# Kernel tuning notes

Hardware: AMD Instinct MI355X
Metric: run time of the kernel (lower is better)

Reference implementation:

```python
import jax, jax.numpy as jnp
import numpy as np

D = 2          # matrix dimension
N = 5_000_000  # chain length (and divisor in I + A_i/n)


def setup_inputs() -> dict:
    key = jax.random.key(0)
    A = jax.random.normal(key, (N, D, D), dtype=jnp.float32)
    return {"A": A}


def reference(A):
    # X = prod_{i=0}^{n-1} (I + A_i / n), left-to-right, exactly as the torch loop.
    n = A.shape[0]
    d = A.shape[1]
    I = jnp.eye(d, dtype=A.dtype)

    def step(X, A_i):
        return X @ (I + A_i / n), None

    X, _ = jax.lax.scan(step, I, A)
    return X
```

## Files before the change

kernel.cpp:

```cpp
#include <hip/hip_runtime.h>


struct M2 { double a, b, c, d; };

__device__ __forceinline__ M2 m2mul(const M2& X, const M2& Y) {
    M2 r;
    r.a = fma(X.a, Y.a, X.b * Y.c);
    r.b = fma(X.a, Y.b, X.b * Y.d);
    r.c = fma(X.c, Y.a, X.d * Y.c);
    r.d = fma(X.c, Y.b, X.d * Y.d);
    return r;
}

__device__ __forceinline__ M2 from_f4(float4 v, double inv_n) {
    M2 M;
    M.a = fma((double)v.x, inv_n, 1.0);
    M.b = (double)v.y * inv_n;
    M.c = (double)v.z * inv_n;
    M.d = fma((double)v.w, inv_n, 1.0);
    return M;
}

__device__ __forceinline__ M2 wave_combine(M2 P) {
    #pragma unroll
    for (int off = 1; off < 64; off <<= 1) {
        M2 Q;
        Q.a = __shfl_down(P.a, off);
        Q.b = __shfl_down(P.b, off);
        Q.c = __shfl_down(P.c, off);
        Q.d = __shfl_down(P.d, off);
        P = m2mul(P, Q);
    }
    return P;
}

__device__ __forceinline__ M2 load_m2(const double* p) {
    double2 lo = *reinterpret_cast<const double2*>(p);
    double2 hi = *reinterpret_cast<const double2*>(p + 2);
    M2 Q = { lo.x, lo.y, hi.x, hi.y };
    return Q;
}

__device__ __forceinline__ void store_m2(double* p, const M2& P) {
    *reinterpret_cast<double2*>(p)     = double2{ P.a, P.b };
    *reinterpret_cast<double2*>(p + 2) = double2{ P.c, P.d };
}

#define CHUNK 5
#define P1_TPB 256
#define WTILE (64 * CHUNK)
#define TILE (P1_TPB * CHUNK)

__global__ void __launch_bounds__(P1_TPB) prodchain_phase1(
    const float4* __restrict__ A, int n, double* __restrict__ part)
{
    __shared__ float4 tile[TILE];
    __shared__ double bl[4 * 4];
    const int tid = threadIdx.x;
    const int w = tid >> 6;
    const int l = tid & 63;
    const int blockStart = blockIdx.x * TILE;
    const int waveStart = blockStart + w * WTILE;
    const double inv_n = 1.0 / (double)n;

    float4* lbase = &tile[w * WTILE];

    if (blockStart + TILE <= n) {
        const float4* gbase = A + waveStart;
        #pragma unroll
        for (int k = 0; k < CHUNK; ++k) {
            __builtin_amdgcn_global_load_lds(
                (const __attribute__((address_space(1))) void*)(gbase + k * 64 + l),
                (__attribute__((address_space(3))) void*)(lbase + k * 64),
                16, 0, 0);
        }
        asm volatile("s_waitcnt vmcnt(0)" ::: "memory");
    } else {
        #pragma unroll
        for (int k = 0; k < CHUNK; ++k) {
            int g = waveStart + k * 64 + l;
            float4 v = (g < n) ? A[g] : make_float4(0.f, 0.f, 0.f, 0.f);
            lbase[k * 64 + l] = v;
        }
    }

    M2 P = {1.0, 0.0, 0.0, 1.0};
    const float4* my = &lbase[l * CHUNK];
    #pragma unroll
    for (int j = 0; j < CHUNK; ++j)
        P = m2mul(P, from_f4(my[j], inv_n));

    P = wave_combine(P);

    if (l == 0) {
        bl[4 * w + 0] = P.a;
        bl[4 * w + 1] = P.b;
        bl[4 * w + 2] = P.c;
        bl[4 * w + 3] = P.d;
    }
    __syncthreads();

    if (tid == 0) {
        M2 R = { bl[0], bl[1], bl[2], bl[3] };
        #pragma unroll
        for (int w2 = 1; w2 < 4; ++w2) {
            M2 Q = { bl[4 * w2 + 0], bl[4 * w2 + 1],
                     bl[4 * w2 + 2], bl[4 * w2 + 3] };
            R = m2mul(R, Q);
        }
        store_m2(&part[4 * blockIdx.x], R);
    }
}

__global__ void __launch_bounds__(64) prodchain_reduce(
    const double* __restrict__ in_part, int np, double* __restrict__ out_part)
{
    const int l = threadIdx.x;
    const int idx = blockIdx.x * 64 + l;
    M2 P = {1.0, 0.0, 0.0, 1.0};
    if (idx < np) P = load_m2(&in_part[4 * idx]);

    P = wave_combine(P);

    if (l == 0) store_m2(&out_part[4 * blockIdx.x], P);
}

__global__ void __launch_bounds__(64) prodchain_final(
    const double* __restrict__ in_part, int np, float* __restrict__ out)
{
    const int l = threadIdx.x;
    M2 P = {1.0, 0.0, 0.0, 1.0};
    if (l < np) P = load_m2(&in_part[4 * l]);

    P = wave_combine(P);

    if (l == 0) {
        out[0] = (float)P.a;
        out[1] = (float)P.b;
        out[2] = (float)P.c;
        out[3] = (float)P.d;
    }
}

extern "C" void kernel_launch(void* const* d_in, const int* in_sizes, int n_in,
                              void* d_out, int out_size, void* d_ws, size_t ws_size,
                              hipStream_t stream) {
    const float4* A = (const float4*)d_in[0];
    const int n = in_sizes[0] / 4;
    const int nb1 = (n + TILE - 1) / TILE;
    const int nb2 = (nb1 + 63) / 64;

    double* part1 = (double*)d_ws;
    double* part2 = part1 + 4 * 4096;

    prodchain_phase1<<<nb1, P1_TPB, 0, stream>>>(A, n, part1);
    prodchain_reduce<<<nb2, 64, 0, stream>>>(part1, nb1, part2);
    prodchain_final<<<1, 64, 0, stream>>>(part2, nb2, (float*)d_out);
}
```

Before: 23.18 us.

## Process two segments per wave, overlapping second load with first compute

Each wave now loads two consecutive 320-element segments into LDS. It waits only for the first batch (vmcnt(5)) before computing that segment's product, so the second batch's load overlaps that arithmetic. The block tile doubles, which halves the number of phase-1 blocks and partials. The small block-reduction scratch is aliased onto the tile buffer behind an extra barrier. The trade-off is fewer blocks in flight for hiding memory latency, plus a second wave-level combine per wave.

```diff
diff --git a/kernel.cpp b/kernel.cpp
--- a/kernel.cpp
+++ b/kernel.cpp
@@ -48,55 +48,85 @@
 
 #define CHUNK 5
 #define P1_TPB 256
-#define WTILE (64 * CHUNK)
-#define TILE (P1_TPB * CHUNK)
+#define SEG (64 * CHUNK)
+#define TILE (SEG * 8)
 
 __global__ void __launch_bounds__(P1_TPB) prodchain_phase1(
     const float4* __restrict__ A, int n, double* __restrict__ part)
 {
     __shared__ float4 tile[TILE];
-    __shared__ double bl[4 * 4];
+    double* bl = (double*)tile;
+
     const int tid = threadIdx.x;
     const int w = tid >> 6;
     const int l = tid & 63;
     const int blockStart = blockIdx.x * TILE;
-    const int waveStart = blockStart + w * WTILE;
+    const int segA = blockStart + (2 * w) * SEG;
+    const int segB = segA + SEG;
     const double inv_n = 1.0 / (double)n;
 
-    float4* lbase = &tile[w * WTILE];
+    float4* la = &tile[(2 * w) * SEG];
+    float4* lb = la + SEG;
 
-    if (blockStart + TILE <= n) {
-        const float4* gbase = A + waveStart;
+    const bool full = (blockStart + TILE <= n);
+    if (full) {
+        const float4* ga = A + segA;
+        const float4* gb = A + segB;
         #pragma unroll
-        for (int k = 0; k < CHUNK; ++k) {
+        for (int k = 0; k < CHUNK; ++k)
             __builtin_amdgcn_global_load_lds(
-                (const __attribute__((address_space(1))) void*)(gbase + k * 64 + l),
-                (__attribute__((address_space(3))) void*)(lbase + k * 64),
+                (const __attribute__((address_space(1))) void*)(ga + k * 64 + l),
+                (__attribute__((address_space(3))) void*)(la + k * 64),
                 16, 0, 0);
-        }
-        asm volatile("s_waitcnt vmcnt(0)" ::: "memory");
+        #pragma unroll
+        for (int k = 0; k < CHUNK; ++k)
+            __builtin_amdgcn_global_load_lds(
+                (const __attribute__((address_space(1))) void*)(gb + k * 64 + l),
+                (__attribute__((address_space(3))) void*)(lb + k * 64),
+                16, 0, 0);
+        asm volatile("s_waitcnt vmcnt(5)" ::: "memory");
     } else {
         #pragma unroll
         for (int k = 0; k < CHUNK; ++k) {
-            int g = waveStart + k * 64 + l;
-            float4 v = (g < n) ? A[g] : make_float4(0.f, 0.f, 0.f, 0.f);
-            lbase[k * 64 + l] = v;
+            int g = segA + k * 64 + l;
+            la[k * 64 + l] = (g < n) ? A[g] : make_float4(0.f, 0.f, 0.f, 0.f);
         }
+        #pragma unroll
+        for (int k = 0; k < CHUNK; ++k) {
+            int g = segB + k * 64 + l;
+            lb[k * 64 + l] = (g < n) ? A[g] : make_float4(0.f, 0.f, 0.f, 0.f);
+        }
+        asm volatile("s_waitcnt lgkmcnt(0)" ::: "memory");
     }
 
     M2 P = {1.0, 0.0, 0.0, 1.0};
-    const float4* my = &lbase[l * CHUNK];
-    #pragma unroll
-    for (int j = 0; j < CHUNK; ++j)
-        P = m2mul(P, from_f4(my[j], inv_n));
+    {
+        const float4* my = &la[l * CHUNK];
+        #pragma unroll
+        for (int j = 0; j < CHUNK; ++j)
+            P = m2mul(P, from_f4(my[j], inv_n));
+    }
+
+    if (full) asm volatile("s_waitcnt vmcnt(0)" ::: "memory");
+
+    M2 Q = {1.0, 0.0, 0.0, 1.0};
+    {
+        const float4* my = &lb[l * CHUNK];
+        #pragma unroll
+        for (int j = 0; j < CHUNK; ++j)
+            Q = m2mul(Q, from_f4(my[j], inv_n));
+    }
 
     P = wave_combine(P);
+    Q = wave_combine(Q);
 
+    __syncthreads();
     if (l == 0) {
-        bl[4 * w + 0] = P.a;
-        bl[4 * w + 1] = P.b;
-        bl[4 * w + 2] = P.c;
-        bl[4 * w + 3] = P.d;
+        M2 R = m2mul(P, Q);
+        bl[4 * w + 0] = R.a;
+        bl[4 * w + 1] = R.b;
+        bl[4 * w + 2] = R.c;
+        bl[4 * w + 3] = R.d;
     }
     __syncthreads();
 
@@ -104,9 +134,9 @@
         M2 R = { bl[0], bl[1], bl[2], bl[3] };
         #pragma unroll
         for (int w2 = 1; w2 < 4; ++w2) {
-            M2 Q = { bl[4 * w2 + 0], bl[4 * w2 + 1],
+            M2 T = { bl[4 * w2 + 0], bl[4 * w2 + 1],
                      bl[4 * w2 + 2], bl[4 * w2 + 3] };
-            R = m2mul(R, Q);
+            R = m2mul(R, T);
         }
         store_m2(&part[4 * blockIdx.x], R);
     }
@@ -151,7 +181,7 @@
     const int nb2 = (nb1 + 63) / 64;
 
     double* part1 = (double*)d_ws;
-    double* part2 = part1 + 4 * 4096;
+    double* part2 = part1 + 4 * 2048;
 
     prodchain_phase1<<<nb1, P1_TPB, 0, stream>>>(A, n, part1);
     prodchain_reduce<<<nb2, 64, 0, stream>>>(part1, nb1, part2);
```

Result: slower. 23.71 us (+2.3%).

## Fuse three-stage product reduction into one kernel with last-block atomic counters

Applied to the files above, without the earlier changes.

Merges the phase1, reduce and final kernels into a single kernel. Each group's last-arriving block, found via an atomic counter, reduces that group's partials, and the last group finisher computes the final product. This removes two kernel launches and their inter-kernel gaps but adds a memset of the counters and relies on relaxed atomics with waitcnt for cross-block visibility, which risks memory-ordering issues.

```diff
diff --git a/kernel.cpp b/kernel.cpp
--- a/kernel.cpp
+++ b/kernel.cpp
@@ -34,16 +34,20 @@
     return P;
 }
 
-__device__ __forceinline__ M2 load_m2(const double* p) {
-    double2 lo = *reinterpret_cast<const double2*>(p);
-    double2 hi = *reinterpret_cast<const double2*>(p + 2);
-    M2 Q = { lo.x, lo.y, hi.x, hi.y };
+__device__ __forceinline__ M2 load_m2_sc1(const double* p) {
+    M2 Q;
+    Q.a = __hip_atomic_load(p + 0, __ATOMIC_RELAXED, __HIP_MEMORY_SCOPE_AGENT);
+    Q.b = __hip_atomic_load(p + 1, __ATOMIC_RELAXED, __HIP_MEMORY_SCOPE_AGENT);
+    Q.c = __hip_atomic_load(p + 2, __ATOMIC_RELAXED, __HIP_MEMORY_SCOPE_AGENT);
+    Q.d = __hip_atomic_load(p + 3, __ATOMIC_RELAXED, __HIP_MEMORY_SCOPE_AGENT);
     return Q;
 }
 
-__device__ __forceinline__ void store_m2(double* p, const M2& P) {
-    *reinterpret_cast<double2*>(p)     = double2{ P.a, P.b };
-    *reinterpret_cast<double2*>(p + 2) = double2{ P.c, P.d };
+__device__ __forceinline__ void store_m2_sc1(double* p, const M2& P) {
+    __hip_atomic_store(p + 0, P.a, __ATOMIC_RELAXED, __HIP_MEMORY_SCOPE_AGENT);
+    __hip_atomic_store(p + 1, P.b, __ATOMIC_RELAXED, __HIP_MEMORY_SCOPE_AGENT);
+    __hip_atomic_store(p + 2, P.c, __ATOMIC_RELAXED, __HIP_MEMORY_SCOPE_AGENT);
+    __hip_atomic_store(p + 3, P.d, __ATOMIC_RELAXED, __HIP_MEMORY_SCOPE_AGENT);
 }
 
 #define CHUNK 5
@@ -51,11 +55,14 @@
 #define WTILE (64 * CHUNK)
 #define TILE (P1_TPB * CHUNK)
 
-__global__ void __launch_bounds__(P1_TPB) prodchain_phase1(
-    const float4* __restrict__ A, int n, double* __restrict__ part)
+__global__ void __launch_bounds__(P1_TPB) prodchain_fused(
+    const float4* __restrict__ A, int n, int nb, int ng,
+    double* __restrict__ part, double* __restrict__ gpart,
+    unsigned* __restrict__ cnt, float* __restrict__ out)
 {
     __shared__ float4 tile[TILE];
     __shared__ double bl[4 * 4];
+    __shared__ int role;
     const int tid = threadIdx.x;
     const int w = tid >> 6;
     const int l = tid & 63;
@@ -79,16 +86,18 @@
         #pragma unroll
         for (int k = 0; k < CHUNK; ++k) {
             int g = waveStart + k * 64 + l;
-            float4 v = (g < n) ? A[g] : make_float4(0.f, 0.f, 0.f, 0.f);
-            lbase[k * 64 + l] = v;
+            lbase[k * 64 + l] = (g < n) ? A[g] : make_float4(0.f, 0.f, 0.f, 0.f);
         }
+        asm volatile("s_waitcnt lgkmcnt(0)" ::: "memory");
     }
 
     M2 P = {1.0, 0.0, 0.0, 1.0};
-    const float4* my = &lbase[l * CHUNK];
-    #pragma unroll
-    for (int j = 0; j < CHUNK; ++j)
-        P = m2mul(P, from_f4(my[j], inv_n));
+    {
+        const float4* my = &lbase[l * CHUNK];
+        #pragma unroll
+        for (int j = 0; j < CHUNK; ++j)
+            P = m2mul(P, from_f4(my[j], inv_n));
+    }
 
     P = wave_combine(P);
 
@@ -100,6 +109,7 @@
     }
     __syncthreads();
 
+    const int grp = blockIdx.x >> 6;
     if (tid == 0) {
         M2 R = { bl[0], bl[1], bl[2], bl[3] };
         #pragma unroll
@@ -108,37 +118,49 @@
                      bl[4 * w2 + 2], bl[4 * w2 + 3] };
             R = m2mul(R, Q);
         }
-        store_m2(&part[4 * blockIdx.x], R);
+        store_m2_sc1(&part[4 * blockIdx.x], R);
+        asm volatile("s_waitcnt vmcnt(0)" ::: "memory");
+        unsigned members = (unsigned)min(64, nb - (grp << 6));
+        unsigned old = __hip_atomic_fetch_add(&cnt[grp], 1u, __ATOMIC_RELAXED,
+                                              __HIP_MEMORY_SCOPE_AGENT);
+        role = (old == members - 1) ? 1 : 0;
     }
-}
+    __syncthreads();
 
-__global__ void __launch_bounds__(64) prodchain_reduce(
-    const double* __restrict__ in_part, int np, double* __restrict__ out_part)
-{
-    const int l = threadIdx.x;
-    const int idx = blockIdx.x * 64 + l;
-    M2 P = {1.0, 0.0, 0.0, 1.0};
-    if (idx < np) P = load_m2(&in_part[4 * idx]);
+    if (!role) return;
 
-    P = wave_combine(P);
+    if (tid < 64) {
+        int idx = (grp << 6) + l;
+        M2 T = {1.0, 0.0, 0.0, 1.0};
+        if (idx < nb) T = load_m2_sc1(&part[4 * idx]);
+        T = wave_combine(T);
 
-    if (l == 0) store_m2(&out_part[4 * blockIdx.x], P);
-}
+        int fin = 0;
+        if (l == 0) {
+            store_m2_sc1(&gpart[4 * grp], T);
+            asm volatile("s_waitcnt vmcnt(0)" ::: "memory");
+            unsigned old2 = __hip_atomic_fetch_add(&cnt[ng], 1u, __ATOMIC_RELAXED,
+                                                   __HIP_MEMORY_SCOPE_AGENT);
+            fin = (old2 == (unsigned)ng - 1) ? 1 : 0;
+        }
+        fin = __shfl(fin, 0);
 
-__global__ void __launch_bounds__(64) prodchain_final(
-    const double* __restrict__ in_part, int np, float* __restrict__ out)
-{
-    const int l = threadIdx.x;
-    M2 P = {1.0, 0.0, 0.0, 1.0};
-    if (l < np) P = load_m2(&in_part[4 * l]);
-
-    P = wave_combine(P);
-
-    if (l == 0) {
-        out[0] = (float)P.a;
-        out[1] = (float)P.b;
-        out[2] = (float)P.c;
-        out[3] = (float)P.d;
+        if (fin) {
+            M2 F = {1.0, 0.0, 0.0, 1.0};
+            for (int p = 0; p * 64 < ng; ++p) {
+                int gi = p * 64 + l;
+                M2 T2 = {1.0, 0.0, 0.0, 1.0};
+                if (gi < ng) T2 = load_m2_sc1(&gpart[4 * gi]);
+                T2 = wave_combine(T2);
+                F = m2mul(F, T2);
+            }
+            if (l == 0) {
+                out[0] = (float)F.a;
+                out[1] = (float)F.b;
+                out[2] = (float)F.c;
+                out[3] = (float)F.d;
+            }
+        }
     }
 }
 
@@ -147,13 +169,14 @@
                               hipStream_t stream) {
     const float4* A = (const float4*)d_in[0];
     const int n = in_sizes[0] / 4;
-    const int nb1 = (n + TILE - 1) / TILE;
-    const int nb2 = (nb1 + 63) / 64;
+    const int nb = (n + TILE - 1) / TILE;
+    const int ng = (nb + 63) / 64;
 
-    double* part1 = (double*)d_ws;
-    double* part2 = part1 + 4 * 4096;
+    double*   part  = (double*)d_ws;
+    unsigned* cnt   = (unsigned*)((char*)d_ws + 126976);
+    double*   gpart = (double*)((char*)d_ws + 131072);
 
-    prodchain_phase1<<<nb1, P1_TPB, 0, stream>>>(A, n, part1);
-    prodchain_reduce<<<nb2, 64, 0, stream>>>(part1, nb1, part2);
-    prodchain_final<<<1, 64, 0, stream>>>(part2, nb2, (float*)d_out);
+    hipMemsetAsync(cnt, 0, (ng + 1) * sizeof(unsigned), stream);
+    prodchain_fused<<<nb, P1_TPB, 0, stream>>>(A, n, nb, ng, part, gpart,
+                                               cnt, (float*)d_out);
 }
```

New measurement: 52.39 us. 2.26x slower.

## Fuse reduce and final kernels using last-block atomic counter

Applied to the files above, without the earlier changes.

Merges the second-level reduce and the final single-block kernel into one tail kernel. Each block publishes its partial with agent-scope stores and bumps an atomic counter, and the last block to arrive combines all group partials and writes the output. This removes one kernel launch and its inter-kernel gap, but adds a memset node to reset the counter on every call, so the launch count stays the same. It also adds a small lgkmcnt wait in the tail-load path.

```diff
diff --git a/kernel.cpp b/kernel.cpp
--- a/kernel.cpp
+++ b/kernel.cpp
@@ -46,6 +46,22 @@
     *reinterpret_cast<double2*>(p + 2) = double2{ P.c, P.d };
 }
 
+__device__ __forceinline__ M2 load_m2_sc1(const double* p) {
+    M2 Q;
+    Q.a = __hip_atomic_load(p + 0, __ATOMIC_RELAXED, __HIP_MEMORY_SCOPE_AGENT);
+    Q.b = __hip_atomic_load(p + 1, __ATOMIC_RELAXED, __HIP_MEMORY_SCOPE_AGENT);
+    Q.c = __hip_atomic_load(p + 2, __ATOMIC_RELAXED, __HIP_MEMORY_SCOPE_AGENT);
+    Q.d = __hip_atomic_load(p + 3, __ATOMIC_RELAXED, __HIP_MEMORY_SCOPE_AGENT);
+    return Q;
+}
+
+__device__ __forceinline__ void store_m2_sc1(double* p, const M2& P) {
+    __hip_atomic_store(p + 0, P.a, __ATOMIC_RELAXED, __HIP_MEMORY_SCOPE_AGENT);
+    __hip_atomic_store(p + 1, P.b, __ATOMIC_RELAXED, __HIP_MEMORY_SCOPE_AGENT);
+    __hip_atomic_store(p + 2, P.c, __ATOMIC_RELAXED, __HIP_MEMORY_SCOPE_AGENT);
+    __hip_atomic_store(p + 3, P.d, __ATOMIC_RELAXED, __HIP_MEMORY_SCOPE_AGENT);
+}
+
 #define CHUNK 5
 #define P1_TPB 256
 #define WTILE (64 * CHUNK)
@@ -79,9 +95,9 @@
         #pragma unroll
         for (int k = 0; k < CHUNK; ++k) {
             int g = waveStart + k * 64 + l;
-            float4 v = (g < n) ? A[g] : make_float4(0.f, 0.f, 0.f, 0.f);
-            lbase[k * 64 + l] = v;
+            lbase[k * 64 + l] = (g < n) ? A[g] : make_float4(0.f, 0.f, 0.f, 0.f);
         }
+        asm volatile("s_waitcnt lgkmcnt(0)" ::: "memory");
     }
 
     M2 P = {1.0, 0.0, 0.0, 1.0};
@@ -112,33 +128,37 @@
     }
 }
 
-__global__ void __launch_bounds__(64) prodchain_reduce(
-    const double* __restrict__ in_part, int np, double* __restrict__ out_part)
+__global__ void __launch_bounds__(64) prodchain_tail(
+    const double* __restrict__ part, int np, int ng,
+    double* __restrict__ gpart, unsigned* __restrict__ cnt,
+    float* __restrict__ out)
 {
     const int l = threadIdx.x;
     const int idx = blockIdx.x * 64 + l;
     M2 P = {1.0, 0.0, 0.0, 1.0};
-    if (idx < np) P = load_m2(&in_part[4 * idx]);
+    if (idx < np) P = load_m2(&part[4 * idx]);
 
     P = wave_combine(P);
 
-    if (l == 0) store_m2(&out_part[4 * blockIdx.x], P);
-}
+    int fin = 0;
+    if (l == 0) {
+        store_m2_sc1(&gpart[4 * blockIdx.x], P);
+        asm volatile("s_waitcnt vmcnt(0)" ::: "memory");
+        unsigned old = __hip_atomic_fetch_add(cnt, 1u, __ATOMIC_RELAXED,
+                                              __HIP_MEMORY_SCOPE_AGENT);
+        fin = (old == (unsigned)ng - 1) ? 1 : 0;
+    }
+    fin = __shfl(fin, 0);
+    if (!fin) return;
 
-__global__ void __launch_bounds__(64) prodchain_final(
-    const double* __restrict__ in_part, int np, float* __restrict__ out)
-{
-    const int l = threadIdx.x;
-    M2 P = {1.0, 0.0, 0.0, 1.0};
-    if (l < np) P = load_m2(&in_part[4 * l]);
-
-    P = wave_combine(P);
-
+    M2 F = {1.0, 0.0, 0.0, 1.0};
+    if (l < ng) F = load_m2_sc1(&gpart[4 * l]);
+    F = wave_combine(F);
     if (l == 0) {
-        out[0] = (float)P.a;
-        out[1] = (float)P.b;
-        out[2] = (float)P.c;
-        out[3] = (float)P.d;
+        out[0] = (float)F.a;
+        out[1] = (float)F.b;
+        out[2] = (float)F.c;
+        out[3] = (float)F.d;
     }
 }
 
@@ -148,12 +168,14 @@
     const float4* A = (const float4*)d_in[0];
     const int n = in_sizes[0] / 4;
     const int nb1 = (n + TILE - 1) / TILE;
-    const int nb2 = (nb1 + 63) / 64;
+    const int ng = (nb1 + 63) / 64;
 
-    double* part1 = (double*)d_ws;
-    double* part2 = part1 + 4 * 4096;
+    double*   part  = (double*)d_ws;
+    double*   gpart = (double*)((char*)d_ws + 131072);
+    unsigned* cnt   = (unsigned*)((char*)d_ws + 135168);
 
-    prodchain_phase1<<<nb1, P1_TPB, 0, stream>>>(A, n, part1);
-    prodchain_reduce<<<nb2, 64, 0, stream>>>(part1, nb1, part2);
-    prodchain_final<<<1, 64, 0, stream>>>(part2, nb2, (float*)d_out);
+    hipMemsetAsync(cnt, 0, sizeof(unsigned), stream);
+    prodchain_phase1<<<nb1, P1_TPB, 0, stream>>>(A, n, part);
+    prodchain_tail<<<ng, 64, 0, stream>>>(part, nb1, ng, gpart, cnt,
+                                          (float*)d_out);
 }
```

New measurement: 28.30 us. 1.22x slower.
